# Optimization experiments

Measured on AMD Instinct MI355X. Metric: run time of the kernel, lower is better.

## Reference

```python
import jax, jax.numpy as jnp
import numpy as np

T, N, E, C = 16, 20000, 320000, 128
EPS = 1e-5


def setup_inputs() -> dict:
    key = jax.random.key(0)
    ks = jax.random.split(key, 6)
    x = jax.random.normal(ks[0], (T, N, C), dtype=jnp.float32)
    edge_index = jax.random.randint(ks[1], (2, E), 0, N, dtype=jnp.int32)
    edge_weight = jax.random.uniform(ks[2], (E,), dtype=jnp.float32)
    # temporal Conv1d weight [out, in, k=3], scaled like torch default init
    Wt = jax.random.normal(ks[3], (C, C, 3), dtype=jnp.float32) * (1.0 / np.sqrt(C * 3))
    bt = jnp.zeros((C,), dtype=jnp.float32)
    # GCNConv linear weight [out, in] (no bias) + separate aggregation bias
    Wg = jax.random.normal(ks[4], (C, C), dtype=jnp.float32) * (1.0 / np.sqrt(C))
    bg = jnp.zeros((C,), dtype=jnp.float32)
    gamma = jnp.ones((C,), dtype=jnp.float32)
    beta = jnp.zeros((C,), dtype=jnp.float32)
    return {"x": x, "edge_index": edge_index, "edge_weight": edge_weight,
            "Wt": Wt, "bt": bt, "Wg": Wg, "bg": bg, "gamma": gamma, "beta": beta}


def _forward(x, edge_index, edge_weight, Wt, bt, Wg, bg, gamma, beta):
    # temporal conv: treat nodes as batch -> [N, C, T]
    xc = jnp.transpose(x, (1, 2, 0))
    h = jax.lax.conv_general_dilated(xc, Wt, window_strides=(1,),
                                     padding=[(1, 1)],
                                     dimension_numbers=("NCH", "OIH", "NCH"))
    h = h + bt[None, :, None]
    h = jnp.transpose(h, (2, 0, 1))  # [T, N, C]

    # GCN normalization with self-loops (fill_value=1.0)
    loops = jnp.arange(N, dtype=edge_index.dtype)
    src = jnp.concatenate([edge_index[0], loops])
    dst = jnp.concatenate([edge_index[1], loops])
    w = jnp.concatenate([edge_weight, jnp.ones((N,), edge_weight.dtype)])
    deg = jax.ops.segment_sum(w, dst, num_segments=N)
    dinv = jnp.where(deg > 0, jax.lax.rsqrt(jnp.maximum(deg, 1e-12)), 0.0)
    norm = dinv[src] * w * dinv[dst]  # [E+N]

    def step(carry, x_t):
        ht = x_t @ Wg.T                                 # [N, C]
        msg = ht[src] * norm[:, None]                   # [E+N, C]
        agg = jax.ops.segment_sum(msg, dst, num_segments=N) + bg
        mu = agg.mean(axis=0)
        var = jnp.mean((agg - mu) ** 2, axis=0)         # biased, training BN
        y = gamma * (agg - mu) * jax.lax.rsqrt(var + EPS) + beta
        return carry, jax.nn.relu(y)

    _, out = jax.lax.scan(step, None, h)  # [T, N, C]
    return out


def reference(x, edge_index, edge_weight, Wt, bt, Wg, bg, gamma, beta):
    return _forward(x, edge_index, edge_weight, Wt, bt, Wg, bg, gamma, beta)
```

## Files before the change

kernel.cpp:

```cpp
#include <hip/hip_runtime.h>
#include <cstdint>

#define TT 16
#define NN 20000
#define CC 128
#define EE 320000
#define KKDIM 384
#define EPSV 1e-5f

typedef unsigned short u16;
typedef u16 u16x4 __attribute__((ext_vector_type(4)));
typedef u16 u16x8 __attribute__((ext_vector_type(8)));
typedef __bf16 bf16x8 __attribute__((ext_vector_type(8)));
typedef float f32x4 __attribute__((ext_vector_type(4)));

static __device__ __forceinline__ u16 f2bf(float f) {
  union { float f; uint32_t u; } v; v.f = f;
  uint32_t u = v.u;
  return (u16)((u + 0x7FFFu + ((u >> 16) & 1u)) >> 16);
}
static __device__ __forceinline__ float bf2f(u16 h) {
  union { uint32_t u; float f; } v; v.u = ((uint32_t)h) << 16;
  return v.f;
}
static __device__ __forceinline__ uint32_t cvtpk(float lo, float hi) {
  uint32_t r;
  asm volatile("v_cvt_pk_bf16_f32 %0, %1, %2" : "=v"(r) : "v"(lo), "v"(hi));
  return r;
}

__global__ __launch_bounds__(384) void k_prepw(const float* __restrict__ Wt,
                                               const float* __restrict__ bt,
                                               const float* __restrict__ Wg,
                                               u16* __restrict__ BmatT,
                                               float* __restrict__ b2) {
  const int o = blockIdx.x;
  const int kk = threadIdx.x;
  const int k = kk >> 7, i = kk & 127;
  float acc = 0.f;
  for (int c = 0; c < CC; ++c)
    acc += Wg[o * CC + c] * Wt[(size_t)c * 384 + i * 3 + k];
  BmatT[(size_t)o * KKDIM + kk] = f2bf(acc);
  if (kk == 0) {
    float b = 0.f;
    for (int c = 0; c < CC; ++c) b += Wg[o * CC + c] * bt[c];
    b2[o] = b;
  }
}

__global__ __launch_bounds__(256) void k_deginit(float* __restrict__ deg,
                                                 int* __restrict__ cnt) {
  int n = blockIdx.x * 256 + threadIdx.x;
  if (n < NN) { deg[n] = 1.0f; cnt[n] = 1; }
}
__global__ __launch_bounds__(256) void k_count(const int* __restrict__ ei,
                                               const float* __restrict__ ew,
                                               float* __restrict__ deg,
                                               int* __restrict__ cnt) {
  int e = blockIdx.x * 256 + threadIdx.x;
  if (e >= EE) return;
  int d = ei[EE + e];
  atomicAdd(&deg[d], ew[e]);
  atomicAdd(&cnt[d], 1);
}
__global__ __launch_bounds__(256) void k_dinv(float* __restrict__ deg) {
  int n = blockIdx.x * 256 + threadIdx.x;
  if (n >= NN) return;
  float d = deg[n];
  deg[n] = (d > 0.f) ? rsqrtf(fmaxf(d, 1e-12f)) : 0.f;
}

__global__ __launch_bounds__(1024) void k_scan(const int* __restrict__ cnt,
                                               int* __restrict__ rowptr) {
  __shared__ int part[1024];
  const int tid = threadIdx.x;
  const int base = tid * 20;
  int s = 0;
  for (int j = 0; j < 20; ++j) {
    int idx = base + j;
    if (idx < NN) s += cnt[idx];
  }
  part[tid] = s;
  __syncthreads();
  for (int off = 1; off < 1024; off <<= 1) {
    int u = 0;
    if (tid >= off) u = part[tid - off];
    __syncthreads();
    part[tid] += u;
    __syncthreads();
  }
  int run = part[tid] - s;
  for (int j = 0; j < 20; ++j) {
    int idx = base + j;
    if (idx < NN) { rowptr[idx] = run; run += cnt[idx]; }
  }
  if (tid == 1023) rowptr[NN] = part[1023];
}

__global__ __launch_bounds__(256) void k_scatter(const int* __restrict__ ei,
                                                 const float* __restrict__ ew,
                                                 const int* __restrict__ rowptr,
                                                 int* __restrict__ fill,
                                                 const float* __restrict__ dinv,
                                                 int2* __restrict__ cw) {
  int e = blockIdx.x * 256 + threadIdx.x;
  if (e < EE) {
    int s = ei[e], d = ei[EE + e];
    int pos = rowptr[d] + atomicAdd(&fill[d], 1);
    cw[pos] = make_int2(s, __float_as_int(dinv[s] * ew[e] * dinv[d]));
  } else if (e < EE + NN) {
    int n = e - EE;
    float dn = dinv[n];
    int pos = rowptr[n] + atomicAdd(&fill[n], 1);
    cw[pos] = make_int2(n, __float_as_int(dn * dn));
  }
}

__global__ __launch_bounds__(256) void k_conv(const float* __restrict__ x,
                                              const u16* __restrict__ BmatT,
                                              const float* __restrict__ b2,
                                              u16* __restrict__ ht) {
  __shared__ __align__(16) u16 As[128][72];
  __shared__ __align__(16) u16 Bs[128][72];
  const int t = blockIdx.y;
  const int row0 = blockIdx.x * 128;
  const int tid = threadIdx.x;
  const int lane = tid & 63;
  const int wv = tid >> 6;

  f32x4 acc[2][8];
  for (int m = 0; m < 2; ++m)
    for (int nb = 0; nb < 8; ++nb) acc[m][nb] = (f32x4){0.f, 0.f, 0.f, 0.f};

  const int r0 = tid >> 4;
  const int c4 = tid & 15;

  for (int kt = 0; kt < 6; ++kt) {
    const int kTap = kt >> 1;
    const int i0 = (kt & 1) * 64;
    const int tk = t + kTap - 1;
    const bool tkv = (tk >= 0) && (tk < TT);
    #pragma unroll
    for (int j = 0; j < 8; ++j) {
      const int r = r0 + j * 16;
      const int grow = row0 + r;
      float4 v = make_float4(0.f, 0.f, 0.f, 0.f);
      if (tkv && grow < NN)
        v = *(const float4*)(x + ((size_t)tk * NN + grow) * CC + i0 + c4 * 4);
      uint32_t pk0 = cvtpk(v.x, v.y);
      uint32_t pk1 = cvtpk(v.z, v.w);
      *(uint32_t*)&As[r][c4 * 4] = pk0;
      *(uint32_t*)&As[r][c4 * 4 + 2] = pk1;
    }
    #pragma unroll
    for (int j = 0; j < 4; ++j) {
      const int idx = tid + j * 256;
      const int col = idx >> 3, q = idx & 7;
      *(u16x8*)&Bs[col][q * 8] =
          *(const u16x8*)(BmatT + (size_t)col * KKDIM + kt * 64 + q * 8);
    }
    __syncthreads();
    #pragma unroll
    for (int ks = 0; ks < 2; ++ks) {
      const int k0 = ks * 32 + ((lane >> 4) << 3);
      bf16x8 a0 = __builtin_bit_cast(bf16x8, *(const u16x8*)&As[wv * 32 + (lane & 15)][k0]);
      bf16x8 a1 = __builtin_bit_cast(bf16x8, *(const u16x8*)&As[wv * 32 + 16 + (lane & 15)][k0]);
      #pragma unroll
      for (int nb = 0; nb < 8; ++nb) {
        bf16x8 b = __builtin_bit_cast(bf16x8, *(const u16x8*)&Bs[nb * 16 + (lane & 15)][k0]);
        acc[0][nb] = __builtin_amdgcn_mfma_f32_16x16x32_bf16(a0, b, acc[0][nb], 0, 0, 0);
        acc[1][nb] = __builtin_amdgcn_mfma_f32_16x16x32_bf16(a1, b, acc[1][nb], 0, 0, 0);
      }
    }
    __syncthreads();
  }
  float b2v[8];
  #pragma unroll
  for (int nb = 0; nb < 8; ++nb) b2v[nb] = b2[nb * 16 + (lane & 15)];
  const int rb = row0 + wv * 32 + ((lane >> 4) << 2);
  #pragma unroll
  for (int m = 0; m < 2; ++m)
    #pragma unroll
    for (int nb = 0; nb < 8; ++nb)
      #pragma unroll
      for (int j = 0; j < 4; ++j) {
        const int r = rb + m * 16 + j;
        if (r < NN)
          ht[(size_t)r * 2048 + t * 128 + nb * 16 + (lane & 15)] =
              f2bf(acc[m][nb][j] + b2v[nb]);
      }
}

__global__ __launch_bounds__(256) void k_agg(const u16* __restrict__ ht,
                                             const int2* __restrict__ cw,
                                             const int* __restrict__ rowptr,
                                             u16* __restrict__ agg) {
  const int n = blockIdx.x;
  const int tid = threadIdx.x;
  const int wv = tid >> 6, lane = tid & 63;
  const int tb = wv * 4;
  const int o0 = tb * 128 + lane * 4;
  const int o1 = o0 + 256;
  float acc[2][4] = {{0.f,0.f,0.f,0.f},{0.f,0.f,0.f,0.f}};
  const int beg = rowptr[n], end = rowptr[n + 1];
  int p = beg;
  #define GATHER(ei_, vi_)                                              \
    {                                                                   \
      const u16* rr = ht + (size_t)(ei_).x * 2048;                      \
      vi_[0] = *(const u16x4*)(rr + o0);                                \
      vi_[1] = *(const u16x4*)(rr + o1);                                \
    }
  #define ACCUM(ei_, vi_)                                               \
    {                                                                   \
      const float w_ = __int_as_float((ei_).y);                         \
      _Pragma("unroll") for (int j = 0; j < 2; ++j)                     \
          _Pragma("unroll") for (int k = 0; k < 4; ++k)                 \
              acc[j][k] = fmaf(bf2f(vi_[j][k]), w_, acc[j][k]);         \
    }
  for (; p + 8 <= end; p += 8) {
    int2 e0 = cw[p],     e1 = cw[p + 1], e2 = cw[p + 2], e3 = cw[p + 3];
    int2 e4 = cw[p + 4], e5 = cw[p + 5], e6 = cw[p + 6], e7 = cw[p + 7];
    u16x4 v0[2], v1[2], v2[2], v3[2], v4[2], v5[2], v6[2], v7[2];
    GATHER(e0, v0) GATHER(e1, v1) GATHER(e2, v2) GATHER(e3, v3)
    GATHER(e4, v4) GATHER(e5, v5) GATHER(e6, v6) GATHER(e7, v7)
    ACCUM(e0, v0) ACCUM(e1, v1) ACCUM(e2, v2) ACCUM(e3, v3)
    ACCUM(e4, v4) ACCUM(e5, v5) ACCUM(e6, v6) ACCUM(e7, v7)
  }
  for (; p + 2 <= end; p += 2) {
    int2 e0 = cw[p], e1 = cw[p + 1];
    u16x4 v0[2], v1[2];
    GATHER(e0, v0) GATHER(e1, v1)
    ACCUM(e0, v0) ACCUM(e1, v1)
  }
  if (p < end) {
    int2 e0 = cw[p];
    u16x4 v0[2];
    GATHER(e0, v0)
    ACCUM(e0, v0)
  }
  #undef GATHER
  #undef ACCUM
  u16* dst = agg + (size_t)n * 2048;
  u16x4 s0, s1;
  #pragma unroll
  for (int k = 0; k < 4; ++k) { s0[k] = f2bf(acc[0][k]); s1[k] = f2bf(acc[1][k]); }
  *(u16x4*)(dst + o0) = s0;
  *(u16x4*)(dst + o1) = s1;
}

__global__ __launch_bounds__(256) void k_stats(const u16* __restrict__ agg,
                                               float* __restrict__ stats) {
  const int tid = threadIdx.x;
  const int c = tid & 127, th = tid >> 7;
  float s[8], q[8];
  #pragma unroll
  for (int j = 0; j < 8; ++j) { s[j] = 0.f; q[j] = 0.f; }
  const int nbeg = blockIdx.x * 100, nend = nbeg + 100;
  for (int n = nbeg; n < nend; ++n) {
    const u16* row = agg + (size_t)n * 2048 + c;
    #pragma unroll
    for (int j = 0; j < 8; ++j) {
      float v = bf2f(row[(th * 8 + j) * 128]);
      s[j] += v; q[j] += v * v;
    }
  }
  #pragma unroll
  for (int j = 0; j < 8; ++j) {
    const int t = th * 8 + j;
    atomicAdd(&stats[t * 256 + c], s[j]);
    atomicAdd(&stats[t * 256 + 128 + c], q[j]);
  }
}

__global__ __launch_bounds__(256) void k_fin(const float* __restrict__ stats,
                                             const float* __restrict__ gamma,
                                             const float* __restrict__ beta,
                                             float* __restrict__ scsh) {
  const int idx = blockIdx.x * 256 + threadIdx.x;
  const int t = idx >> 7, c = idx & 127;
  const float inv_n = 1.f / (float)NN;
  float mu = stats[t * 256 + c] * inv_n;
  float var = stats[t * 256 + 128 + c] * inv_n - mu * mu;
  float sc = gamma[c] * rsqrtf(var + EPSV);
  scsh[t * 256 + c] = sc;
  scsh[t * 256 + 128 + c] = beta[c] - sc * mu;
}

__global__ __launch_bounds__(256) void k_norm(const u16* __restrict__ agg,
                                              const float* __restrict__ scsh,
                                              float* __restrict__ out) {
  const int n = blockIdx.x;
  const int tid = threadIdx.x;
  const int c = tid & 127, th = tid >> 7;
  const u16* row = agg + (size_t)n * 2048 + c;
  #pragma unroll
  for (int j = 0; j < 8; ++j) {
    const int t = th * 8 + j;
    float v = bf2f(row[t * 128]);
    float sc = scsh[t * 256 + c];
    float sh = scsh[t * 256 + 128 + c];
    out[(size_t)t * (NN * CC) + (size_t)n * CC + c] = fmaxf(fmaf(v, sc, sh), 0.f);
  }
}

extern "C" void kernel_launch(void* const* d_in, const int* in_sizes, int n_in,
                              void* d_out, int out_size, void* d_ws, size_t ws_size,
                              hipStream_t stream) {
  const float* x     = (const float*)d_in[0];
  const int*   ei    = (const int*)d_in[1];
  const float* ew    = (const float*)d_in[2];
  const float* Wt    = (const float*)d_in[3];
  const float* bt    = (const float*)d_in[4];
  const float* Wg    = (const float*)d_in[5];
  const float* gamma = (const float*)d_in[7];
  const float* beta  = (const float*)d_in[8];
  float* out = (float*)d_out;
  char* ws = (char*)d_ws;

  const size_t off_cnt    = 0;
  const size_t off_fill   = 80000;
  const size_t off_stats  = 160000;
  const size_t zero_bytes = 176384;
  const size_t off_deg    = 176384;
  const size_t off_rowptr = 256384;
  const size_t off_cw     = 336400;
  const size_t off_BmatT  = 3056400;
  const size_t off_b2     = 3154704;
  const size_t off_scsh   = 3155216;
  const size_t off_ht     = 3171600;
  const size_t off_agg    = 85091600;

  int*   cnt    = (int*)(ws + off_cnt);
  int*   fill   = (int*)(ws + off_fill);
  float* stats  = (float*)(ws + off_stats);
  float* deg    = (float*)(ws + off_deg);
  int*   rowptr = (int*)(ws + off_rowptr);
  int2*  cw     = (int2*)(ws + off_cw);
  u16*   BmatT  = (u16*)(ws + off_BmatT);
  float* b2     = (float*)(ws + off_b2);
  float* scsh   = (float*)(ws + off_scsh);
  u16*   ht     = (u16*)(ws + off_ht);
  u16*   agg    = (u16*)(ws + off_agg);

  hipMemsetAsync(ws, 0, zero_bytes, stream);
  k_prepw<<<dim3(CC), dim3(384), 0, stream>>>(Wt, bt, Wg, BmatT, b2);
  k_deginit<<<dim3((NN + 255) / 256), dim3(256), 0, stream>>>(deg, cnt);
  k_count<<<dim3((EE + 255) / 256), dim3(256), 0, stream>>>(ei, ew, deg, cnt);
  k_dinv<<<dim3((NN + 255) / 256), dim3(256), 0, stream>>>(deg);
  k_scan<<<dim3(1), dim3(1024), 0, stream>>>(cnt, rowptr);
  k_scatter<<<dim3((EE + NN + 255) / 256), dim3(256), 0, stream>>>(ei, ew, rowptr,
                                                                   fill, deg, cw);
  const int mtiles = (NN + 127) / 128;
  k_conv<<<dim3(mtiles, TT), dim3(256), 0, stream>>>(x, BmatT, b2, ht);
  k_agg<<<dim3(NN), dim3(256), 0, stream>>>(ht, cw, rowptr, agg);
  k_stats<<<dim3(NN / 100), dim3(256), 0, stream>>>(agg, stats);
  k_fin<<<dim3(8), dim3(256), 0, stream>>>(stats, gamma, beta, scsh);
  k_norm<<<dim3(NN), dim3(256), 0, stream>>>(agg, scsh, out);
}
```

Before: 543.4 us.

## Remap conv and aggregation blocks so each XCD touches a disjoint slice

The conv kernel now uses a flattened 1D grid. Block IDs are remapped so each of the 8 XCDs handles a contiguous range of row tiles across all timesteps, and excess blocks return early. The aggregation kernel now gives each block a single group of 2 timesteps (256 channels×time) for 4 nodes, one wave per node. Since block IDs interleave across XCDs, each XCD gathers only its own slice of ht rows, which improves L2 locality for the random neighbor gathers. The cost is that each wave now issues one 8-byte load per edge instead of two, and the cw edge list is read 8 times as often.

```diff
diff --git a/kernel.cpp b/kernel.cpp
--- a/kernel.cpp
+++ b/kernel.cpp
@@ -120,10 +120,15 @@
                                               const u16* __restrict__ BmatT,
                                               const float* __restrict__ b2,
                                               u16* __restrict__ ht) {
+  const int bid = blockIdx.x;
+  const int xcd = bid & 7;
+  const int s = bid >> 3;
+  const int tile = xcd * 20 + (s % 20);
+  const int t = s / 20;
+  if (tile >= 157) return;
   __shared__ __align__(16) u16 As[128][72];
   __shared__ __align__(16) u16 Bs[128][72];
-  const int t = blockIdx.y;
-  const int row0 = blockIdx.x * 128;
+  const int row0 = tile * 128;
   const int tid = threadIdx.x;
   const int lane = tid & 63;
   const int wv = tid >> 6;
@@ -195,57 +200,44 @@
                                              const int2* __restrict__ cw,
                                              const int* __restrict__ rowptr,
                                              u16* __restrict__ agg) {
-  const int n = blockIdx.x;
-  const int tid = threadIdx.x;
-  const int wv = tid >> 6, lane = tid & 63;
-  const int tb = wv * 4;
-  const int o0 = tb * 128 + lane * 4;
-  const int o1 = o0 + 256;
-  float acc[2][4] = {{0.f,0.f,0.f,0.f},{0.f,0.f,0.f,0.f}};
+  const int bid = blockIdx.x;
+  const int tg = bid & 7;
+  const int wv = threadIdx.x >> 6, lane = threadIdx.x & 63;
+  const int n = (bid >> 3) * 4 + wv;
+  const int o0 = tg * 256 + lane * 4;
+  float acc[4] = {0.f, 0.f, 0.f, 0.f};
   const int beg = rowptr[n], end = rowptr[n + 1];
   int p = beg;
-  #define GATHER(ei_, vi_)                                              \
-    {                                                                   \
-      const u16* rr = ht + (size_t)(ei_).x * 2048;                      \
-      vi_[0] = *(const u16x4*)(rr + o0);                                \
-      vi_[1] = *(const u16x4*)(rr + o1);                                \
-    }
-  #define ACCUM(ei_, vi_)                                               \
-    {                                                                   \
-      const float w_ = __int_as_float((ei_).y);                         \
-      _Pragma("unroll") for (int j = 0; j < 2; ++j)                     \
-          _Pragma("unroll") for (int k = 0; k < 4; ++k)                 \
-              acc[j][k] = fmaf(bf2f(vi_[j][k]), w_, acc[j][k]);         \
-    }
   for (; p + 8 <= end; p += 8) {
     int2 e0 = cw[p],     e1 = cw[p + 1], e2 = cw[p + 2], e3 = cw[p + 3];
     int2 e4 = cw[p + 4], e5 = cw[p + 5], e6 = cw[p + 6], e7 = cw[p + 7];
-    u16x4 v0[2], v1[2], v2[2], v3[2], v4[2], v5[2], v6[2], v7[2];
-    GATHER(e0, v0) GATHER(e1, v1) GATHER(e2, v2) GATHER(e3, v3)
-    GATHER(e4, v4) GATHER(e5, v5) GATHER(e6, v6) GATHER(e7, v7)
-    ACCUM(e0, v0) ACCUM(e1, v1) ACCUM(e2, v2) ACCUM(e3, v3)
-    ACCUM(e4, v4) ACCUM(e5, v5) ACCUM(e6, v6) ACCUM(e7, v7)
-  }
-  for (; p + 2 <= end; p += 2) {
-    int2 e0 = cw[p], e1 = cw[p + 1];
-    u16x4 v0[2], v1[2];
-    GATHER(e0, v0) GATHER(e1, v1)
-    ACCUM(e0, v0) ACCUM(e1, v1)
-  }
-  if (p < end) {
-    int2 e0 = cw[p];
-    u16x4 v0[2];
-    GATHER(e0, v0)
-    ACCUM(e0, v0)
-  }
-  #undef GATHER
-  #undef ACCUM
-  u16* dst = agg + (size_t)n * 2048;
-  u16x4 s0, s1;
-  #pragma unroll
-  for (int k = 0; k < 4; ++k) { s0[k] = f2bf(acc[0][k]); s1[k] = f2bf(acc[1][k]); }
-  *(u16x4*)(dst + o0) = s0;
-  *(u16x4*)(dst + o1) = s1;
+    u16x4 v0 = *(const u16x4*)(ht + (size_t)e0.x * 2048 + o0);
+    u16x4 v1 = *(const u16x4*)(ht + (size_t)e1.x * 2048 + o0);
+    u16x4 v2 = *(const u16x4*)(ht + (size_t)e2.x * 2048 + o0);
+    u16x4 v3 = *(const u16x4*)(ht + (size_t)e3.x * 2048 + o0);
+    u16x4 v4 = *(const u16x4*)(ht + (size_t)e4.x * 2048 + o0);
+    u16x4 v5 = *(const u16x4*)(ht + (size_t)e5.x * 2048 + o0);
+    u16x4 v6 = *(const u16x4*)(ht + (size_t)e6.x * 2048 + o0);
+    u16x4 v7 = *(const u16x4*)(ht + (size_t)e7.x * 2048 + o0);
+    #define ACC1(e_, v_)                                              \
+      {                                                               \
+        const float w_ = __int_as_float((e_).y);                      \
+        _Pragma("unroll") for (int k = 0; k < 4; ++k)                 \
+            acc[k] = fmaf(bf2f((v_)[k]), w_, acc[k]);                 \
+      }
+    ACC1(e0, v0) ACC1(e1, v1) ACC1(e2, v2) ACC1(e3, v3)
+    ACC1(e4, v4) ACC1(e5, v5) ACC1(e6, v6) ACC1(e7, v7)
+  }
+  for (; p < end; ++p) {
+    int2 e = cw[p];
+    u16x4 v = *(const u16x4*)(ht + (size_t)e.x * 2048 + o0);
+    ACC1(e, v)
+  }
+  #undef ACC1
+  u16x4 sv;
+  #pragma unroll
+  for (int k = 0; k < 4; ++k) sv[k] = f2bf(acc[k]);
+  *(u16x4*)(agg + (size_t)n * 2048 + o0) = sv;
 }
 
 __global__ __launch_bounds__(256) void k_stats(const u16* __restrict__ agg,
@@ -350,9 +342,8 @@
   k_scan<<<dim3(1), dim3(1024), 0, stream>>>(cnt, rowptr);
   k_scatter<<<dim3((EE + NN + 255) / 256), dim3(256), 0, stream>>>(ei, ew, rowptr,
                                                                    fill, deg, cw);
-  const int mtiles = (NN + 127) / 128;
-  k_conv<<<dim3(mtiles, TT), dim3(256), 0, stream>>>(x, BmatT, b2, ht);
-  k_agg<<<dim3(NN), dim3(256), 0, stream>>>(ht, cw, rowptr, agg);
+  k_conv<<<dim3(2560), dim3(256), 0, stream>>>(x, BmatT, b2, ht);
+  k_agg<<<dim3(40000), dim3(256), 0, stream>>>(ht, cw, rowptr, agg);
   k_stats<<<dim3(NN / 100), dim3(256), 0, stream>>>(agg, stats);
   k_fin<<<dim3(8), dim3(256), 0, stream>>>(stats, gamma, beta, scsh);
   k_norm<<<dim3(NN), dim3(256), 0, stream>>>(agg, scsh, out);
```

New measurement: 511.7 us. 5.8% less time.
